# Kernel optimization log

Hardware: AMD Instinct MI355X
Metric: run time of the kernel (lower is better)

The kernel has to match this reference:

```python
import jax, jax.numpy as jnp
import numpy as np

H, DM, DK, DV, DFF = 8, 512, 64, 64, 2048
B, S = 8, 1024
EPS = 1e-5


def layernorm_global(x):
    # torch nn.LayerNorm(x.size()[1:], elementwise_affine=False): normalize over ALL dims except batch
    mu = jnp.mean(x, axis=(1, 2), keepdims=True)
    var = jnp.var(x, axis=(1, 2), keepdims=True)
    return (x - mu) / jnp.sqrt(var + EPS)


def mha(q_in, k_in, v_in, wq, bq, wk, bk, wv, bv, wo, bo, causal):
    # wq/wk: [h, dk, dmodel], wv: [h, dv, dmodel] (torch Linear weight layout [out,in])
    q = jnp.einsum('bsd,hkd->bhsk', q_in, wq) + bq[None, :, None, :]
    k = jnp.einsum('bsd,hkd->bhsk', k_in, wk) + bk[None, :, None, :]
    v = jnp.einsum('bsd,hvd->bhsv', v_in, wv) + bv[None, :, None, :]
    scores = jnp.einsum('bhqk,bhsk->bhqs', q, k) / np.sqrt(DK).astype(np.float32)
    if causal:
        Sq = q_in.shape[1]
        mask = jnp.triu(jnp.full((Sq, Sq), -jnp.inf, dtype=scores.dtype), k=1)
        scores = scores + mask[None, None, :, :]
    w = jax.nn.softmax(scores, axis=-1)
    attn = jnp.einsum('bhqs,bhsv->bhqv', w, v)  # [b,h,q,dv]
    concat = attn.transpose(0, 2, 1, 3).reshape(q_in.shape[0], q_in.shape[1], H * DV)
    return concat @ wo.T + bo


def setup_inputs() -> dict:
    key = jax.random.key(0)
    ks = jax.random.split(key, 24)
    f = lambda k, shape: (jax.random.normal(k, shape, dtype=jnp.float32) * 0.02)
    inp = {
        'x_enc': jax.random.normal(ks[0], (B, S, DM), dtype=jnp.float32),
        'x_dec': jax.random.normal(ks[1], (B, S, DM), dtype=jnp.float32),
        # masked self-attention params
        'mq_w': f(ks[2], (H, DK, DM)), 'mq_b': f(ks[3], (H, DK)),
        'mk_w': f(ks[4], (H, DK, DM)), 'mk_b': f(ks[5], (H, DK)),
        'mv_w': f(ks[6], (H, DV, DM)), 'mv_b': f(ks[7], (H, DV)),
        'mo_w': f(ks[8], (DM, H * DV)), 'mo_b': f(ks[9], (DM,)),
        # cross-attention params
        'cq_w': f(ks[10], (H, DK, DM)), 'cq_b': f(ks[11], (H, DK)),
        'ck_w': f(ks[12], (H, DK, DM)), 'ck_b': f(ks[13], (H, DK)),
        'cv_w': f(ks[14], (H, DV, DM)), 'cv_b': f(ks[15], (H, DV)),
        'co_w': f(ks[16], (DM, H * DV)), 'co_b': f(ks[17], (DM,)),
        # feedforward params
        'f1_w': f(ks[18], (DFF, DM)), 'f1_b': f(ks[19], (DFF,)),
        'f2_w': f(ks[20], (DM, DFF)), 'f2_b': f(ks[21], (DM,)),
    }
    return inp


def reference(x_enc, x_dec,
              mq_w, mq_b, mk_w, mk_b, mv_w, mv_b, mo_w, mo_b,
              cq_w, cq_b, ck_w, ck_b, cv_w, cv_b, co_w, co_b,
              f1_w, f1_b, f2_w, f2_b):
    # masked self-attention block (dropout = identity at eval)
    x_dec_n = layernorm_global(x_dec)
    sa = mha(x_dec_n, x_dec_n, x_dec_n, mq_w, mq_b, mk_w, mk_b, mv_w, mv_b, mo_w, mo_b, causal=True)
    current = x_dec + sa
    # cross-attention block
    cur_n = layernorm_global(current)
    enc_n = layernorm_global(x_enc)
    ca = mha(cur_n, enc_n, enc_n, cq_w, cq_b, ck_w, ck_b, cv_w, cv_b, co_w, co_b, causal=False)
    result = current + ca
    # feedforward block
    res_n = layernorm_global(result)
    ff = jax.nn.relu(res_n @ f1_w.T + f1_b) @ f2_w.T + f2_b
    return result + ff
```

## Files before the change

kernel.cpp:

```cpp
#include <hip/hip_runtime.h>
#include <cmath>
#include <cstddef>
#include <cstdint>

#define BN   8
#define SN   1024
#define DMN  512
#define HN   8
#define DKN  64
#define DFFN 2048

typedef short           bf16x8   __attribute__((ext_vector_type(8)));
typedef float           f32x4    __attribute__((ext_vector_type(4)));
typedef float           f32x16   __attribute__((ext_vector_type(16)));
typedef unsigned short  ushortx4 __attribute__((ext_vector_type(4)));
typedef unsigned short  ushortx8 __attribute__((ext_vector_type(8)));
typedef unsigned int    uintx4   __attribute__((ext_vector_type(4)));
typedef unsigned short  u16;
typedef unsigned int    u32;

#define ATT_SC 0.18033688011112042f

__device__ __forceinline__ float bf2f(u16 u) {
  return __uint_as_float(((unsigned int)u) << 16);
}
__device__ __forceinline__ u16 f2bf(float f) {
  unsigned int u = __float_as_uint(f);
  u += 0x7FFFu + ((u >> 16) & 1u);
  return (u16)(u >> 16);
}
__device__ __forceinline__ u32 cvtpk_bf16(float lo, float hi) {
  u32 r;
  asm("v_cvt_pk_bf16_f32 %0, %1, %2" : "=v"(r) : "v"(lo), "v"(hi));
  return r;
}
__device__ __forceinline__ void gload_lds16(const u16* gsrc, u16* ldst) {
  __builtin_amdgcn_global_load_lds(
      (const __attribute__((address_space(1))) unsigned int*)gsrc,
      (__attribute__((address_space(3))) unsigned int*)ldst,
      16, 0, 0);
}
__device__ __forceinline__ int xcd_swz(int lid, int nwg) {
  const int cpx = nwg >> 3;
  return (lid & 7) * cpx + (lid >> 3);
}

__global__ __launch_bounds__(256) void cvt_weights(
    const float* p0, const float* p1, const float* p2, const float* p3,
    const float* p4, const float* p5, const float* p6, const float* p7,
    const float* p8, const float* p9, u16* __restrict__ dst) {
  const int gi = blockIdx.x * 256 + threadIdx.x;
  const int idx = gi * 4;
  const float* src; int off;
  if (idx < 2097152) {
    const int t = idx >> 18; off = idx & 262143;
    switch (t) {
      case 0: src = p0; break; case 1: src = p1; break;
      case 2: src = p2; break; case 3: src = p3; break;
      case 4: src = p4; break; case 5: src = p5; break;
      case 6: src = p6; break; default: src = p7; break;
    }
  } else if (idx < 3145728) { src = p8; off = idx - 2097152; }
  else                      { src = p9; off = idx - 3145728; }
  float4 v = *(const float4*)(src + off);
  ushortx4 o;
  o[0] = f2bf(v.x); o[1] = f2bf(v.y); o[2] = f2bf(v.z); o[3] = f2bf(v.w);
  *(ushortx4*)(dst + idx) = o;
}

__global__ __launch_bounds__(256) void pack_bias(const float* a, const float* b,
                                                 const float* c, const float* d,
                                                 const float* e, float* __restrict__ dst) {
  const int t = threadIdx.x;
#pragma unroll
  for (int i = t; i < 512; i += 256) {
    dst[i]        = a[i];
    dst[512 + i]  = b[i];
    dst[1024 + i] = c[i];
    dst[1536 + i] = d[i];
    dst[2048 + i] = e[i];
  }
}

template<bool INBF>
__global__ __launch_bounds__(256) void ln_sum(const void* __restrict__ Xv_,
                                              float2* __restrict__ part) {
  const int g = blockIdx.x, b = blockIdx.y, t = threadIdx.x;
  float s = 0.f, s2 = 0.f;
  if (INBF) {
    const ushortx8* Xv = (const ushortx8*)((const u16*)Xv_ + (size_t)b * (SN * DMN) + (size_t)g * 8192);
#pragma unroll
    for (int it = 0; it < 4; ++it) {
      ushortx8 x = Xv[t + it * 256];
#pragma unroll
      for (int e = 0; e < 8; ++e) { float f = bf2f(x[e]); s += f; s2 += f * f; }
    }
  } else {
    const float4* Xv = (const float4*)((const float*)Xv_ + (size_t)b * (SN * DMN) + (size_t)g * 8192);
#pragma unroll
    for (int it = 0; it < 8; ++it) {
      float4 x = Xv[t + it * 256];
      s  += x.x + x.y + x.z + x.w;
      s2 += x.x*x.x + x.y*x.y + x.z*x.z + x.w*x.w;
    }
  }
  __shared__ float rs[256], rq[256];
  rs[t] = s; rq[t] = s2;
  __syncthreads();
  for (int off = 128; off > 0; off >>= 1) {
    if (t < off) { rs[t] += rs[t + off]; rq[t] += rq[t + off]; }
    __syncthreads();
  }
  if (t == 0) part[b * 64 + g] = make_float2(rs[0], rq[0]);
}

template<bool INBF>
__global__ __launch_bounds__(256) void ln_norm(const void* __restrict__ Xv_,
                                               const float2* __restrict__ part,
                                               u16* __restrict__ Y) {
  const int g = blockIdx.x, b = blockIdx.y, t = threadIdx.x;
  __shared__ float ss[64], sq[64];
  if (t < 64) { float2 p = part[b * 64 + t]; ss[t] = p.x; sq[t] = p.y; }
  __syncthreads();
  float s = 0.f, q = 0.f;
#pragma unroll
  for (int j = 0; j < 64; ++j) { s += ss[j]; q += sq[j]; }
  const float inv_n = 1.f / (float)(SN * DMN);
  const float mu = s * inv_n;
  const float var = q * inv_n - mu * mu;
  const float rstd = rsqrtf(var + 1e-5f);
  const size_t base = (size_t)b * (SN * DMN) + (size_t)g * 8192;
  if (INBF) {
    const ushortx8* Xv = (const ushortx8*)((const u16*)Xv_ + base);
#pragma unroll
    for (int it = 0; it < 4; ++it) {
      ushortx8 x = Xv[t + it * 256];
      ushortx8 o;
#pragma unroll
      for (int e = 0; e < 8; ++e) o[e] = f2bf((bf2f(x[e]) - mu) * rstd);
      *(ushortx8*)(Y + base + (size_t)(t + it * 256) * 8) = o;
    }
  } else {
    const float4* Xv = (const float4*)((const float*)Xv_ + base);
#pragma unroll
    for (int it = 0; it < 8; ++it) {
      float4 x = Xv[t + it * 256];
      ushortx4 o;
      o[0] = f2bf((x.x - mu) * rstd); o[1] = f2bf((x.y - mu) * rstd);
      o[2] = f2bf((x.z - mu) * rstd); o[3] = f2bf((x.w - mu) * rstd);
      *(ushortx4*)(Y + base + (size_t)(t + it * 256) * 4) = o;
    }
  }
}

template<bool RELU, bool RES, bool RESBF, int OMODE, int BM, bool QSC>
__global__ __launch_bounds__(256) void gemm_mfma(const u16* __restrict__ A,
                                                 const u16* __restrict__ W,
                                                 const float* __restrict__ bias,
                                                 const void* __restrict__ resv,
                                                 void* __restrict__ Cv,
                                                 void* __restrict__ Cv2,
                                                 void* __restrict__ Cv3,
                                                 int M, int N, int K) {
  constexpr int MI = BM / 32;
  __shared__ u16 As[BM * 32];
  __shared__ u16 Bs[128 * 32];
  const int t = threadIdx.x;
  const int lane = t & 63, w = t >> 6;
  const int wm = w >> 1, wn = w & 1;

  const int gx = gridDim.x;
  const int lid = xcd_swz(blockIdx.y * gx + blockIdx.x, gx * gridDim.y);
  const int m0 = (lid / gx) * BM, n0 = (lid % gx) * 128;

  f32x4 acc[MI][4];
#pragma unroll
  for (int i = 0; i < MI; ++i)
#pragma unroll
    for (int j = 0; j < 4; ++j)
      acc[i][j] = (f32x4){0.f, 0.f, 0.f, 0.f};

  const int lrow = lane >> 2;
  const int lcol = (lane & 3) * 8;
  const int rofs = (lane & 15) * 32 + (lane >> 4) * 8;

  for (int k0 = 0; k0 < K; k0 += 32) {
    if (BM == 128) {
#pragma unroll
      for (int c = 0; c < 2; ++c) {
        const int r0 = w * 32 + c * 16;
        gload_lds16(A + (size_t)(m0 + r0 + lrow) * K + k0 + lcol, &As[r0 * 32]);
      }
    } else {
      const int r0 = w * 16;
      gload_lds16(A + (size_t)(m0 + r0 + lrow) * K + k0 + lcol, &As[r0 * 32]);
    }
#pragma unroll
    for (int c = 0; c < 2; ++c) {
      const int r0 = w * 32 + c * 16;
      gload_lds16(W + (size_t)(n0 + r0 + lrow) * K + k0 + lcol, &Bs[r0 * 32]);
    }
    __syncthreads();
    bf16x8 af[MI], bfr[4];
#pragma unroll
    for (int f = 0; f < MI; ++f)
      af[f]  = *(const bf16x8*)&As[(wm * (BM / 2) + f * 16) * 32 + rofs];
#pragma unroll
    for (int f = 0; f < 4; ++f)
      bfr[f] = *(const bf16x8*)&Bs[(wn * 64 + f * 16) * 32 + rofs];
#pragma unroll
    for (int i = 0; i < MI; ++i)
#pragma unroll
      for (int j = 0; j < 4; ++j)
        acc[i][j] = __builtin_amdgcn_mfma_f32_16x16x32_bf16(af[i], bfr[j], acc[i][j], 0, 0, 0);
    __syncthreads();
  }

  const int crow0 = (lane >> 4) * 4;
  const int ccol  = lane & 15;
  float bv[4];
#pragma unroll
  for (int j = 0; j < 4; ++j) bv[j] = bias[n0 + wn * 64 + j * 16 + ccol];

  u16* seg_out = nullptr;
  int  seg_n0 = 0;
  bool seg_vt = false;
  if (OMODE == 3) {
    if (n0 < 512)       { seg_out = (u16*)Cv;  seg_n0 = 0; }
    else if (n0 < 1024) { seg_out = (u16*)Cv2; seg_n0 = 512; }
    else                { seg_out = (u16*)Cv3; seg_n0 = 1024; seg_vt = true; }
  } else if (OMODE == 4) {
    if (n0 < 512)       { seg_out = (u16*)Cv;  seg_n0 = 0; }
    else                { seg_out = (u16*)Cv3; seg_n0 = 512; seg_vt = true; }
  }
  const bool do_scale = QSC && (OMODE != 3 || n0 < 512);

#pragma unroll
  for (int i = 0; i < MI; ++i) {
#pragma unroll
    for (int r = 0; r < 4; ++r) {
      const int m = m0 + wm * (BM / 2) + i * 16 + crow0 + r;
#pragma unroll
      for (int j = 0; j < 4; ++j) {
        const int n = n0 + wn * 64 + j * 16 + ccol;
        float v = acc[i][j][r] + bv[j];
        if (RELU) v = fmaxf(v, 0.f);
        if (RES) {
          if (RESBF) v += bf2f(((const u16*)resv)[(size_t)m * N + n]);
          else       v += ((const float*)resv)[(size_t)m * N + n];
        }
        if (do_scale) v *= ATT_SC;
        if (OMODE == 0) {
          ((float*)Cv)[(size_t)m * N + n] = v;
        } else if (OMODE == 1) {
          ((u16*)Cv)[(size_t)m * N + n] = f2bf(v);
        } else {
          const int nn = n - seg_n0;
          if (!seg_vt) seg_out[(size_t)m * 512 + nn] = f2bf(v);
          else
            seg_out[(((size_t)(m >> 10) * HN + (nn >> 6)) * 64 + (nn & 63)) * SN + (m & 1023)] = f2bf(v);
        }
      }
    }
  }
}

#define QBLK 128
#define KVB  64

template<int CAUSAL, int NSPLIT>
__global__ __launch_bounds__(256) void attn_mfma(const u16* __restrict__ Q,
                                                 const u16* __restrict__ K,
                                                 const u16* __restrict__ VT,
                                                 u16* __restrict__ Out,
                                                 float* __restrict__ Lbuf) {
  const int lid = xcd_swz(blockIdx.y * 8 + blockIdx.x, 512);
  const int qb = lid & 7;
  const int bh = lid >> 3;
  const int sp = (NSPLIT > 1) ? blockIdx.z : 0;
  const int b = bh >> 3, h = bh & 7;
  const int t = threadIdx.x;
  const int lane = t & 63, w = t >> 6;
  const int l31 = lane & 31, hi = lane >> 5;

  __shared__ __align__(16) u16 Ks[64 * 64];
  __shared__ __align__(16) u16 Vts[8 * 512];

  const int qw0 = qb * QBLK + w * 32;
  const int qglob = qw0 + l31;

  bf16x8 bq[4];
#pragma unroll
  for (int dk = 0; dk < 4; ++dk)
    bq[dk] = *(const bf16x8*)(Q + (size_t)(b * SN + qglob) * 512
                                + h * 64 + dk * 16 + hi * 8);

  f32x16 acc0 = {}, acc1 = {};
  float l_run = 0.f;

  const int ntile = CAUSAL ? (2 * qb + 2) : (SN / KVB);
  const int n4 = (ntile + NSPLIT - 1) / NSPLIT;
  const int kt0 = sp * n4;
  const int ktend = (kt0 + n4 < ntile) ? (kt0 + n4) : ntile;

  const int srow = t >> 2;
  const int ss0  = 2 * (t & 3);
  const u16* kg0 = K + (size_t)(b * SN + srow) * 512 + h * 64 + ((ss0 ^ (srow & 7)) * 8);
  const u16* kg1 = K + (size_t)(b * SN + srow) * 512 + h * 64 + (((ss0 + 1) ^ (srow & 7)) * 8);
  u16* kd0 = &Ks[t * 16];
  u16* kd1 = &Ks[t * 16 + 8];
  const int vd = t & 63, vp = t >> 6;
  const u16* vg = VT + ((size_t)bh * 64 + vd) * SN + vp * 16;
  u16* vdst0 = &Vts[(2 * vp) * 512 + vd * 8];
  u16* vdst1 = &Vts[(2 * vp + 1) * 512 + vd * 8];

  ushortx8 kr0, kr1, vr0, vr1;
  {
    const size_t ka = (size_t)kt0 * KVB * 512;
    kr0 = *(const ushortx8*)(kg0 + ka);
    kr1 = *(const ushortx8*)(kg1 + ka);
    vr0 = *(const ushortx8*)(vg + kt0 * KVB);
    vr1 = *(const ushortx8*)(vg + kt0 * KVB + 8);
  }

  for (int kt = kt0; kt < ktend; ++kt) {
    const int k0 = kt * KVB;
    __syncthreads();
    *(ushortx8*)kd0 = kr0;
    *(ushortx8*)kd1 = kr1;
    *(ushortx8*)vdst0 = vr0;
    *(ushortx8*)vdst1 = vr1;
    if (kt + 1 < ktend) {
      const size_t kadv = (size_t)(kt + 1) * KVB * 512;
      kr0 = *(const ushortx8*)(kg0 + kadv);
      kr1 = *(const ushortx8*)(kg1 + kadv);
      vr0 = *(const ushortx8*)(vg + (kt + 1) * KVB);
      vr1 = *(const ushortx8*)(vg + (kt + 1) * KVB + 8);
    }
    __syncthreads();

    if (CAUSAL && k0 > qw0 + 31) continue;

    f32x16 s0 = {}, s1 = {};
    __builtin_amdgcn_s_setprio(1);
#pragma unroll
    for (int dk = 0; dk < 4; ++dk) {
      const int boff = dk * 32 + hi * 16;
      const int sw = boff ^ ((l31 & 7) << 4);
      bf16x8 a0 = *(const bf16x8*)&Ks[l31 * 64 + (sw >> 1)];
      bf16x8 a1 = *(const bf16x8*)&Ks[(32 + l31) * 64 + (sw >> 1)];
      s0 = __builtin_amdgcn_mfma_f32_32x32x16_bf16(a0, bq[dk], s0, 0, 0, 0);
      s1 = __builtin_amdgcn_mfma_f32_32x32x16_bf16(a1, bq[dk], s1, 0, 0, 0);
    }
    __builtin_amdgcn_s_setprio(0);

    if (CAUSAL && (k0 + KVB - 1 > qw0)) {
#pragma unroll
      for (int i = 0; i < 16; ++i) {
        const int krow = (i & 3) + 8 * (i >> 2) + 4 * hi;
        if (k0 + krow > qglob)      s0[i] = -INFINITY;
        if (k0 + 32 + krow > qglob) s1[i] = -INFINITY;
      }
    }
    float ps = 0.f;
#pragma unroll
    for (int i = 0; i < 16; ++i) {
      s0[i] = exp2f(s0[i]); ps += s0[i];
      s1[i] = exp2f(s1[i]); ps += s1[i];
    }
    l_run += ps;

    __builtin_amdgcn_s_setprio(1);
#pragma unroll
    for (int ksb = 0; ksb < 4; ++ksb) {
      const int kb = ksb & 1;
      u32 A0, A1, B0, B1;
      if (ksb < 2) {
        A0 = cvtpk_bf16(s0[8*kb + 0], s0[8*kb + 1]);
        A1 = cvtpk_bf16(s0[8*kb + 2], s0[8*kb + 3]);
        B0 = cvtpk_bf16(s0[8*kb + 4], s0[8*kb + 5]);
        B1 = cvtpk_bf16(s0[8*kb + 6], s0[8*kb + 7]);
      } else {
        A0 = cvtpk_bf16(s1[8*kb + 0], s1[8*kb + 1]);
        A1 = cvtpk_bf16(s1[8*kb + 2], s1[8*kb + 3]);
        B0 = cvtpk_bf16(s1[8*kb + 4], s1[8*kb + 5]);
        B1 = cvtpk_bf16(s1[8*kb + 6], s1[8*kb + 7]);
      }
      const u32 xA0 = __shfl_xor(A0, 32), xA1 = __shfl_xor(A1, 32);
      const u32 xB0 = __shfl_xor(B0, 32), xB1 = __shfl_xor(B1, 32);
      uintx4 pw;
      pw[0] = hi ? xB0 : A0;
      pw[1] = hi ? xB1 : A1;
      pw[2] = hi ? B0 : xA0;
      pw[3] = hi ? B1 : xA1;
      const bf16x8 pb = *(const bf16x8*)&pw;
      const bf16x8 av0 = *(const bf16x8*)&Vts[(ksb * 2 + hi) * 512 + l31 * 8];
      const bf16x8 av1 = *(const bf16x8*)&Vts[(ksb * 2 + hi) * 512 + (32 + l31) * 8];
      acc0 = __builtin_amdgcn_mfma_f32_32x32x16_bf16(av0, pb, acc0, 0, 0, 0);
      acc1 = __builtin_amdgcn_mfma_f32_32x32x16_bf16(av1, pb, acc1, 0, 0, 0);
    }
    __builtin_amdgcn_s_setprio(0);
  }

  l_run += __shfl_xor(l_run, 32);
  u16* op = Out + (((size_t)(sp * 64 + bh)) * 1024 + qglob) * 64;
#pragma unroll
  for (int g = 0; g < 4; ++g) {
    ushortx4 o0, o1;
#pragma unroll
    for (int r = 0; r < 4; ++r) {
      o0[r] = f2bf(acc0[4*g + r]);
      o1[r] = f2bf(acc1[4*g + r]);
    }
    *(ushortx4*)(op + 4*hi + 8*g)      = o0;
    *(ushortx4*)(op + 32 + 4*hi + 8*g) = o1;
  }
  if (hi == 0)
    Lbuf[((size_t)(sp * 64 + bh)) * 1024 + qglob] = l_run;
}

__global__ __launch_bounds__(256) void attn_merge2(const u16* __restrict__ Pacc,
                                                   const float* __restrict__ Lbuf,
                                                   u16* __restrict__ O) {
  const int tid = blockIdx.x * 256 + threadIdx.x;
  const int qh = tid >> 3;
  const int d0 = (tid & 7) * 8;
  const int bh = qh >> 10, q = qh & 1023;
  const int b = bh >> 3, h = bh & 7;

  const float l = Lbuf[(size_t)bh * 1024 + q] + Lbuf[(size_t)(64 + bh) * 1024 + q];
  const float inv = 1.f / l;
  ushortx8 a0 = *(const ushortx8*)(Pacc + ((size_t)bh * 1024 + q) * 64 + d0);
  ushortx8 a1 = *(const ushortx8*)(Pacc + ((size_t)(64 + bh) * 1024 + q) * 64 + d0);
  ushortx8 ov;
#pragma unroll
  for (int e = 0; e < 8; ++e)
    ov[e] = f2bf((bf2f(a0[e]) + bf2f(a1[e])) * inv);
  *(ushortx8*)(O + ((size_t)(b * 1024 + q) * 512) + h * 64 + d0) = ov;
}

extern "C" void kernel_launch(void* const* d_in, const int* in_sizes, int n_in,
                              void* d_out, int out_size, void* d_ws, size_t ws_size,
                              hipStream_t stream) {
  const float* x_enc = (const float*)d_in[0];
  const float* x_dec = (const float*)d_in[1];
  const float* mq_w = (const float*)d_in[2];  const float* mq_b = (const float*)d_in[3];
  const float* mk_w = (const float*)d_in[4];  const float* mk_b = (const float*)d_in[5];
  const float* mv_w = (const float*)d_in[6];  const float* mv_b = (const float*)d_in[7];
  const float* mo_w = (const float*)d_in[8];  const float* mo_b = (const float*)d_in[9];
  const float* cq_w = (const float*)d_in[10]; const float* cq_b = (const float*)d_in[11];
  const float* ck_w = (const float*)d_in[12]; const float* ck_b = (const float*)d_in[13];
  const float* cv_w = (const float*)d_in[14]; const float* cv_b = (const float*)d_in[15];
  const float* co_w = (const float*)d_in[16]; const float* co_b = (const float*)d_in[17];
  const float* f1_w = (const float*)d_in[18]; const float* f1_b = (const float*)d_in[19];
  const float* f2_w = (const float*)d_in[20]; const float* f2_b = (const float*)d_in[21];
  float* out = (float*)d_out;

  char* wsb = (char*)d_ws;
  u16* o5    = (u16*)(wsb + 0);
  u16* o6    = (u16*)(wsb + (16u << 20));
  u16* Qb    = (u16*)(wsb + (32u << 20));
  u16* Kb    = (u16*)(wsb + (40u << 20));
  u16* VTb   = (u16*)(wsb + (48u << 20));
  u16* B0    = (u16*)(wsb + (56u << 20));
  u16* B1    = (u16*)(wsb + (64u << 20));
  u16* FF1   = (u16*)(wsb + (72u << 20));
  u16* WB    = (u16*)(wsb + (104u << 20));
  float2* part = (float2*)(wsb + (112u << 20));
  float* BC  = (float*)(wsb + (113u << 20));

  u16* Pacc   = FF1;
  float* Lbuf = (float*)B1;

  u16* wb_mq = WB + 0 * 262144;
  u16* wb_mo = WB + 3 * 262144;
  u16* wb_cq = WB + 4 * 262144;
  u16* wb_ck = WB + 5 * 262144;
  u16* wb_co = WB + 7 * 262144;
  u16* wb_f1 = WB + 8 * 262144; u16* wb_f2 = WB + 8 * 262144 + 1048576;

  const int M = BN * SN;
  dim3 ln_grid(64, BN);
  dim3 g512s(512 / 128, M / 64);
  dim3 g1024(1024 / 128, M / 128);
  dim3 g1536(1536 / 128, M / 128);
  dim3 g2048(2048 / 128, M / 128);
  dim3 attn_grid(SN / QBLK, BN * HN, 2);

  cvt_weights<<<4096, 256, 0, stream>>>(mq_w, mk_w, mv_w, mo_w, cq_w, ck_w, cv_w, co_w,
                                        f1_w, f2_w, WB);
  pack_bias<<<1, 256, 0, stream>>>(mq_b, mk_b, mv_b, ck_b, cv_b, BC);

  ln_sum<false><<<ln_grid, 256, 0, stream>>>(x_dec, part);
  ln_norm<false><<<ln_grid, 256, 0, stream>>>(x_dec, part, B0);
  gemm_mfma<false, false, false, 3, 128, true><<<g1536, 256, 0, stream>>>(B0, wb_mq, BC, nullptr,
                                                                          Qb, Kb, VTb, M, 1536, 512);
  attn_mfma<1, 2><<<attn_grid, 256, 0, stream>>>(Qb, Kb, VTb, Pacc, Lbuf);
  attn_merge2<<<2048, 256, 0, stream>>>(Pacc, Lbuf, B0);
  gemm_mfma<false, true, false, 1, 64, false><<<g512s, 256, 0, stream>>>(B0, wb_mo, mo_b, x_dec,
                                                                         o5, nullptr, nullptr, M, 512, 512);

  ln_sum<true><<<ln_grid, 256, 0, stream>>>(o5, part);
  ln_norm<true><<<ln_grid, 256, 0, stream>>>(o5, part, B0);
  ln_sum<false><<<ln_grid, 256, 0, stream>>>(x_enc, part);
  ln_norm<false><<<ln_grid, 256, 0, stream>>>(x_enc, part, B1);
  gemm_mfma<false, false, false, 1, 64, true><<<g512s, 256, 0, stream>>>(B0, wb_cq, cq_b, nullptr,
                                                                         Qb, nullptr, nullptr, M, 512, 512);
  gemm_mfma<false, false, false, 4, 128, false><<<g1024, 256, 0, stream>>>(B1, wb_ck, BC + 1536, nullptr,
                                                                           Kb, nullptr, VTb, M, 1024, 512);
  attn_mfma<0, 2><<<attn_grid, 256, 0, stream>>>(Qb, Kb, VTb, Pacc, Lbuf);
  attn_merge2<<<2048, 256, 0, stream>>>(Pacc, Lbuf, B0);
  gemm_mfma<false, true, true, 1, 64, false><<<g512s, 256, 0, stream>>>(B0, wb_co, co_b, o5,
                                                                        o6, nullptr, nullptr, M, 512, 512);

  ln_sum<true><<<ln_grid, 256, 0, stream>>>(o6, part);
  ln_norm<true><<<ln_grid, 256, 0, stream>>>(o6, part, B0);
  gemm_mfma<true, false, false, 1, 128, false><<<g2048, 256, 0, stream>>>(B0, wb_f1, f1_b, nullptr,
                                                                          FF1, nullptr, nullptr, M, 2048, 512);
  gemm_mfma<false, true, true, 0, 64, false><<<g512s, 256, 0, stream>>>(FF1, wb_f2, f2_b, o6,
                                                                        out, nullptr, nullptr, M, 512, 2048);
}
```

Before: 286.9 us.

## Fuse dual layernorms, drop split-KV for cross-attention, simplify P register layout

The two back-to-back layernorms of the residual stream and the encoder input are merged into single launches that use a z-dimension. Cross-attention now runs with no KV split and normalizes its output in the epilogue, which removes the merge kernel and the partial-buffer traffic. The P-to-bf16 packing drops the cross-lane shuffles: V is stored to LDS in an interleaved order so that P can stay in its own lanes. K/V pointers are now advanced incrementally. The cost is half as many workgroups for cross-attention, which can lower occupancy and parallelism.

```diff
diff --git a/kernel.cpp b/kernel.cpp
--- a/kernel.cpp
+++ b/kernel.cpp
@@ -83,9 +83,7 @@
 }
 
 template<bool INBF>
-__global__ __launch_bounds__(256) void ln_sum(const void* __restrict__ Xv_,
-                                              float2* __restrict__ part) {
-  const int g = blockIdx.x, b = blockIdx.y, t = threadIdx.x;
+__device__ __forceinline__ void ln_sum_body(const void* Xv_, float2* part, int g, int b, int t) {
   float s = 0.f, s2 = 0.f;
   if (INBF) {
     const ushortx8* Xv = (const ushortx8*)((const u16*)Xv_ + (size_t)b * (SN * DMN) + (size_t)g * 8192);
@@ -115,10 +113,8 @@
 }
 
 template<bool INBF>
-__global__ __launch_bounds__(256) void ln_norm(const void* __restrict__ Xv_,
-                                               const float2* __restrict__ part,
-                                               u16* __restrict__ Y) {
-  const int g = blockIdx.x, b = blockIdx.y, t = threadIdx.x;
+__device__ __forceinline__ void ln_norm_body(const void* Xv_, const float2* part,
+                                             u16* Y, int g, int b, int t) {
   __shared__ float ss[64], sq[64];
   if (t < 64) { float2 p = part[b * 64 + t]; ss[t] = p.x; sq[t] = p.y; }
   __syncthreads();
@@ -151,6 +147,32 @@
       *(ushortx4*)(Y + base + (size_t)(t + it * 256) * 4) = o;
     }
   }
+}
+
+template<bool INBF>
+__global__ __launch_bounds__(256) void ln_sum(const void* __restrict__ Xv_,
+                                              float2* __restrict__ part) {
+  ln_sum_body<INBF>(Xv_, part, blockIdx.x, blockIdx.y, threadIdx.x);
+}
+template<bool INBF>
+__global__ __launch_bounds__(256) void ln_norm(const void* __restrict__ Xv_,
+                                               const float2* __restrict__ part,
+                                               u16* __restrict__ Y) {
+  ln_norm_body<INBF>(Xv_, part, Y, blockIdx.x, blockIdx.y, threadIdx.x);
+}
+__global__ __launch_bounds__(256) void ln_sum2(const void* __restrict__ X0,
+                                               const void* __restrict__ X1,
+                                               float2* __restrict__ part) {
+  if (blockIdx.z == 0) ln_sum_body<true>(X0, part, blockIdx.x, blockIdx.y, threadIdx.x);
+  else                 ln_sum_body<false>(X1, part + 512, blockIdx.x, blockIdx.y, threadIdx.x);
+}
+__global__ __launch_bounds__(256) void ln_norm2(const void* __restrict__ X0,
+                                                const void* __restrict__ X1,
+                                                const float2* __restrict__ part,
+                                                u16* __restrict__ Y0,
+                                                u16* __restrict__ Y1) {
+  if (blockIdx.z == 0) ln_norm_body<true>(X0, part, Y0, blockIdx.x, blockIdx.y, threadIdx.x);
+  else                 ln_norm_body<false>(X1, part + 512, Y1, blockIdx.x, blockIdx.y, threadIdx.x);
 }
 
 template<bool RELU, bool RES, bool RESBF, int OMODE, int BM, bool QSC>
@@ -305,37 +327,45 @@
 
   const int srow = t >> 2;
   const int ss0  = 2 * (t & 3);
-  const u16* kg0 = K + (size_t)(b * SN + srow) * 512 + h * 64 + ((ss0 ^ (srow & 7)) * 8);
-  const u16* kg1 = K + (size_t)(b * SN + srow) * 512 + h * 64 + (((ss0 + 1) ^ (srow & 7)) * 8);
+  const u16* kg0 = K + (size_t)(b * SN + srow) * 512 + h * 64 + ((ss0 ^ (srow & 7)) * 8)
+                     + (size_t)kt0 * KVB * 512;
+  const u16* kg1 = K + (size_t)(b * SN + srow) * 512 + h * 64 + (((ss0 + 1) ^ (srow & 7)) * 8)
+                     + (size_t)kt0 * KVB * 512;
   u16* kd0 = &Ks[t * 16];
   u16* kd1 = &Ks[t * 16 + 8];
   const int vd = t & 63, vp = t >> 6;
-  const u16* vg = VT + ((size_t)bh * 64 + vd) * SN + vp * 16;
+  const u16* vg = VT + ((size_t)bh * 64 + vd) * SN + vp * 16 + kt0 * KVB;
   u16* vdst0 = &Vts[(2 * vp) * 512 + vd * 8];
   u16* vdst1 = &Vts[(2 * vp + 1) * 512 + vd * 8];
 
   ushortx8 kr0, kr1, vr0, vr1;
-  {
-    const size_t ka = (size_t)kt0 * KVB * 512;
-    kr0 = *(const ushortx8*)(kg0 + ka);
-    kr1 = *(const ushortx8*)(kg1 + ka);
-    vr0 = *(const ushortx8*)(vg + kt0 * KVB);
-    vr1 = *(const ushortx8*)(vg + kt0 * KVB + 8);
-  }
+  kr0 = *(const ushortx8*)kg0;
+  kr1 = *(const ushortx8*)kg1;
+  vr0 = *(const ushortx8*)vg;
+  vr1 = *(const ushortx8*)(vg + 8);
+  kg0 += (size_t)KVB * 512; kg1 += (size_t)KVB * 512; vg += KVB;
 
   for (int kt = kt0; kt < ktend; ++kt) {
     const int k0 = kt * KVB;
     __syncthreads();
     *(ushortx8*)kd0 = kr0;
     *(ushortx8*)kd1 = kr1;
-    *(ushortx8*)vdst0 = vr0;
-    *(ushortx8*)vdst1 = vr1;
+    {
+      ushortx8 sl, sh;
+#pragma unroll
+      for (int e = 0; e < 4; ++e) {
+        sl[e] = vr0[e];     sl[e + 4] = vr1[e];
+        sh[e] = vr0[e + 4]; sh[e + 4] = vr1[e + 4];
+      }
+      *(ushortx8*)vdst0 = sl;
+      *(ushortx8*)vdst1 = sh;
+    }
     if (kt + 1 < ktend) {
-      const size_t kadv = (size_t)(kt + 1) * KVB * 512;
-      kr0 = *(const ushortx8*)(kg0 + kadv);
-      kr1 = *(const ushortx8*)(kg1 + kadv);
-      vr0 = *(const ushortx8*)(vg + (kt + 1) * KVB);
-      vr1 = *(const ushortx8*)(vg + (kt + 1) * KVB + 8);
+      kr0 = *(const ushortx8*)kg0;
+      kr1 = *(const ushortx8*)kg1;
+      vr0 = *(const ushortx8*)vg;
+      vr1 = *(const ushortx8*)(vg + 8);
+      kg0 += (size_t)KVB * 512; kg1 += (size_t)KVB * 512; vg += KVB;
     }
     __syncthreads();
 
@@ -372,30 +402,24 @@
 
     __builtin_amdgcn_s_setprio(1);
 #pragma unroll
-    for (int ksb = 0; ksb < 4; ++ksb) {
-      const int kb = ksb & 1;
-      u32 A0, A1, B0, B1;
-      if (ksb < 2) {
-        A0 = cvtpk_bf16(s0[8*kb + 0], s0[8*kb + 1]);
-        A1 = cvtpk_bf16(s0[8*kb + 2], s0[8*kb + 3]);
-        B0 = cvtpk_bf16(s0[8*kb + 4], s0[8*kb + 5]);
-        B1 = cvtpk_bf16(s0[8*kb + 6], s0[8*kb + 7]);
+    for (int m = 0; m < 4; ++m) {
+      uintx4 pw;
+      if (m == 0) {
+        pw[0] = cvtpk_bf16(s0[0], s0[1]);  pw[1] = cvtpk_bf16(s0[2], s0[3]);
+        pw[2] = cvtpk_bf16(s0[4], s0[5]);  pw[3] = cvtpk_bf16(s0[6], s0[7]);
+      } else if (m == 1) {
+        pw[0] = cvtpk_bf16(s0[8], s0[9]);  pw[1] = cvtpk_bf16(s0[10], s0[11]);
+        pw[2] = cvtpk_bf16(s0[12], s0[13]); pw[3] = cvtpk_bf16(s0[14], s0[15]);
+      } else if (m == 2) {
+        pw[0] = cvtpk_bf16(s1[0], s1[1]);  pw[1] = cvtpk_bf16(s1[2], s1[3]);
+        pw[2] = cvtpk_bf16(s1[4], s1[5]);  pw[3] = cvtpk_bf16(s1[6], s1[7]);
       } else {
-        A0 = cvtpk_bf16(s1[8*kb + 0], s1[8*kb + 1]);
-        A1 = cvtpk_bf16(s1[8*kb + 2], s1[8*kb + 3]);
-        B0 = cvtpk_bf16(s1[8*kb + 4], s1[8*kb + 5]);
-        B1 = cvtpk_bf16(s1[8*kb + 6], s1[8*kb + 7]);
-      }
-      const u32 xA0 = __shfl_xor(A0, 32), xA1 = __shfl_xor(A1, 32);
-      const u32 xB0 = __shfl_xor(B0, 32), xB1 = __shfl_xor(B1, 32);
-      uintx4 pw;
-      pw[0] = hi ? xB0 : A0;
-      pw[1] = hi ? xB1 : A1;
-      pw[2] = hi ? B0 : xA0;
-      pw[3] = hi ? B1 : xA1;
+        pw[0] = cvtpk_bf16(s1[8], s1[9]);  pw[1] = cvtpk_bf16(s1[10], s1[11]);
+        pw[2] = cvtpk_bf16(s1[12], s1[13]); pw[3] = cvtpk_bf16(s1[14], s1[15]);
+      }
       const bf16x8 pb = *(const bf16x8*)&pw;
-      const bf16x8 av0 = *(const bf16x8*)&Vts[(ksb * 2 + hi) * 512 + l31 * 8];
-      const bf16x8 av1 = *(const bf16x8*)&Vts[(ksb * 2 + hi) * 512 + (32 + l31) * 8];
+      const bf16x8 av0 = *(const bf16x8*)&Vts[(m * 2 + hi) * 512 + l31 * 8];
+      const bf16x8 av1 = *(const bf16x8*)&Vts[(m * 2 + hi) * 512 + (32 + l31) * 8];
       acc0 = __builtin_amdgcn_mfma_f32_32x32x16_bf16(av0, pb, acc0, 0, 0, 0);
       acc1 = __builtin_amdgcn_mfma_f32_32x32x16_bf16(av1, pb, acc1, 0, 0, 0);
     }
@@ -403,20 +427,36 @@
   }
 
   l_run += __shfl_xor(l_run, 32);
-  u16* op = Out + (((size_t)(sp * 64 + bh)) * 1024 + qglob) * 64;
-#pragma unroll
-  for (int g = 0; g < 4; ++g) {
-    ushortx4 o0, o1;
-#pragma unroll
-    for (int r = 0; r < 4; ++r) {
-      o0[r] = f2bf(acc0[4*g + r]);
-      o1[r] = f2bf(acc1[4*g + r]);
-    }
-    *(ushortx4*)(op + 4*hi + 8*g)      = o0;
-    *(ushortx4*)(op + 32 + 4*hi + 8*g) = o1;
-  }
-  if (hi == 0)
-    Lbuf[((size_t)(sp * 64 + bh)) * 1024 + qglob] = l_run;
+  if (NSPLIT == 1) {
+    const float inv = 1.f / l_run;
+    u16* op = Out + (size_t)(b * SN + qglob) * 512 + h * 64;
+#pragma unroll
+    for (int g = 0; g < 4; ++g) {
+      ushortx4 o0, o1;
+#pragma unroll
+      for (int r = 0; r < 4; ++r) {
+        o0[r] = f2bf(acc0[4*g + r] * inv);
+        o1[r] = f2bf(acc1[4*g + r] * inv);
+      }
+      *(ushortx4*)(op + 4*hi + 8*g)      = o0;
+      *(ushortx4*)(op + 32 + 4*hi + 8*g) = o1;
+    }
+  } else {
+    u16* op = Out + (((size_t)(sp * 64 + bh)) * 1024 + qglob) * 64;
+#pragma unroll
+    for (int g = 0; g < 4; ++g) {
+      ushortx4 o0, o1;
+#pragma unroll
+      for (int r = 0; r < 4; ++r) {
+        o0[r] = f2bf(acc0[4*g + r]);
+        o1[r] = f2bf(acc1[4*g + r]);
+      }
+      *(ushortx4*)(op + 4*hi + 8*g)      = o0;
+      *(ushortx4*)(op + 32 + 4*hi + 8*g) = o1;
+    }
+    if (hi == 0)
+      Lbuf[((size_t)(sp * 64 + bh)) * 1024 + qglob] = l_run;
+  }
 }
 
 __global__ __launch_bounds__(256) void attn_merge2(const u16* __restrict__ Pacc,
@@ -481,11 +521,13 @@
 
   const int M = BN * SN;
   dim3 ln_grid(64, BN);
+  dim3 ln_grid2(64, BN, 2);
   dim3 g512s(512 / 128, M / 64);
   dim3 g1024(1024 / 128, M / 128);
   dim3 g1536(1536 / 128, M / 128);
   dim3 g2048(2048 / 128, M / 128);
-  dim3 attn_grid(SN / QBLK, BN * HN, 2);
+  dim3 attn_grid_c(SN / QBLK, BN * HN, 2);
+  dim3 attn_grid_x(SN / QBLK, BN * HN, 1);
 
   cvt_weights<<<4096, 256, 0, stream>>>(mq_w, mk_w, mv_w, mo_w, cq_w, ck_w, cv_w, co_w,
                                         f1_w, f2_w, WB);
@@ -495,21 +537,18 @@
   ln_norm<false><<<ln_grid, 256, 0, stream>>>(x_dec, part, B0);
   gemm_mfma<false, false, false, 3, 128, true><<<g1536, 256, 0, stream>>>(B0, wb_mq, BC, nullptr,
                                                                           Qb, Kb, VTb, M, 1536, 512);
-  attn_mfma<1, 2><<<attn_grid, 256, 0, stream>>>(Qb, Kb, VTb, Pacc, Lbuf);
+  attn_mfma<1, 2><<<attn_grid_c, 256, 0, stream>>>(Qb, Kb, VTb, Pacc, Lbuf);
   attn_merge2<<<2048, 256, 0, stream>>>(Pacc, Lbuf, B0);
   gemm_mfma<false, true, false, 1, 64, false><<<g512s, 256, 0, stream>>>(B0, wb_mo, mo_b, x_dec,
                                                                          o5, nullptr, nullptr, M, 512, 512);
 
-  ln_sum<true><<<ln_grid, 256, 0, stream>>>(o5, part);
-  ln_norm<true><<<ln_grid, 256, 0, stream>>>(o5, part, B0);
-  ln_sum<false><<<ln_grid, 256, 0, stream>>>(x_enc, part);
-  ln_norm<false><<<ln_grid, 256, 0, stream>>>(x_enc, part, B1);
+  ln_sum2<<<ln_grid2, 256, 0, stream>>>(o5, x_enc, part);
+  ln_norm2<<<ln_grid2, 256, 0, stream>>>(o5, x_enc, part, B0, B1);
   gemm_mfma<false, false, false, 1, 64, true><<<g512s, 256, 0, stream>>>(B0, wb_cq, cq_b, nullptr,
                                                                          Qb, nullptr, nullptr, M, 512, 512);
   gemm_mfma<false, false, false, 4, 128, false><<<g1024, 256, 0, stream>>>(B1, wb_ck, BC + 1536, nullptr,
                                                                            Kb, nullptr, VTb, M, 1024, 512);
-  attn_mfma<0, 2><<<attn_grid, 256, 0, stream>>>(Qb, Kb, VTb, Pacc, Lbuf);
-  attn_merge2<<<2048, 256, 0, stream>>>(Pacc, Lbuf, B0);
+  attn_mfma<0, 1><<<attn_grid_x, 256, 0, stream>>>(Qb, Kb, VTb, B0, nullptr);
   gemm_mfma<false, true, true, 1, 64, false><<<g512s, 256, 0, stream>>>(B0, wb_co, co_b, o5,
                                                                         o6, nullptr, nullptr, M, 512, 512);
 
```

Measured after the change: 271.9 us. -5.2%, faster.
